# Performance work log

Measured on AMD Instinct MI355X. Metric: run time of the kernel, lower is better.

## Reference

```python
import math
import jax, jax.numpy as jnp
import numpy as np

D_MODEL = 1024
N_HEADS = 16
HEAD_DIM = D_MODEL // N_HEADS  # 64
QDIM = HEAD_DIM // 4           # 16
SPIKE_SLOPE = 5.0
B, S = 2, 2048


def _qweight(r, i, j, k):
    # Hamilton-product weight matrix, identical to QLinear.forward's torch.cat construction.
    return jnp.concatenate([
        jnp.concatenate([r, -i, -j, -k], 1),
        jnp.concatenate([i, r, -k, j], 1),
        jnp.concatenate([j, k, r, -i], 1),
        jnp.concatenate([k, -j, i, r], 1),
    ], 0)


def setup_inputs() -> dict:
    key = jax.random.key(0)
    ks = jax.random.split(key, 20)
    Qo = Qi = D_MODEL // 4  # 256
    p = lambda k, shape, s=0.02: (jax.random.normal(k, shape, dtype=jnp.float32) * s)
    inp = {
        'query': jax.random.normal(ks[0], (B, S, D_MODEL), dtype=jnp.float32),
        'key_in': jax.random.normal(ks[1], (B, S, D_MODEL), dtype=jnp.float32),
        'value': jax.random.normal(ks[2], (B, S, D_MODEL), dtype=jnp.float32),
        'mask': jnp.ones((B, S), dtype=jnp.int32),
        'density_feat': jax.random.normal(ks[3], (B, S, 3), dtype=jnp.float32),
        # q_proj QLinear params
        'wq_r': p(ks[4], (Qo, Qi)), 'wq_i': p(ks[5], (Qo, Qi)),
        'wq_j': p(ks[6], (Qo, Qi)), 'wq_k': p(ks[7], (Qo, Qi)),
        'bq': jnp.zeros((D_MODEL,), jnp.float32),
        # k_proj QLinear params
        'wk_r': p(ks[8], (Qo, Qi)), 'wk_i': p(ks[9], (Qo, Qi)),
        'wk_j': p(ks[10], (Qo, Qi)), 'wk_k': p(ks[11], (Qo, Qi)),
        'bk': jnp.zeros((D_MODEL,), jnp.float32),
        # v_proj / out_proj dense params
        'wv': p(ks[12], (D_MODEL, D_MODEL)), 'bv': jnp.zeros((D_MODEL,), jnp.float32),
        'wo': p(ks[13], (D_MODEL, D_MODEL)), 'bo': jnp.zeros((D_MODEL,), jnp.float32),
        # learned spike threshold (init -1.0 as in torch)
        'threshold': jnp.asarray(-1.0, dtype=jnp.float32),
        # density_mod MLP (use nonzero values so the gate shift is exercised)
        'dm1_w': p(ks[14], (16, 3), 0.5), 'dm1_b': p(ks[15], (16,), 0.1),
        'dm2_w': p(ks[16], (1, 16), 0.5), 'dm2_b': p(ks[17], (1,), 0.1),
    }
    return inp


def reference(query, key_in, value, mask, density_feat,
              wq_r, wq_i, wq_j, wq_k, bq,
              wk_r, wk_i, wk_j, wk_k, bk,
              wv, bv, wo, bo, threshold,
              dm1_w, dm1_b, dm2_w, dm2_b):
    H, hd, Qd = N_HEADS, HEAD_DIM, QDIM
    Bq, Sq, D = query.shape

    Wq = _qweight(wq_r, wq_i, wq_j, wq_k)
    Wk = _qweight(wk_r, wk_i, wk_j, wk_k)
    q = query @ Wq.T + bq
    k = key_in @ Wk.T + bk
    v = value @ wv.T + bv

    # head-major split, matching torch.cat(x.split(hd, -1), dim=0)
    qh = q.reshape(Bq, Sq, H, hd).transpose(2, 0, 1, 3)  # (H,B,S,hd)
    kh = k.reshape(Bq, Sq, H, hd).transpose(2, 0, 1, 3)
    vh = v.reshape(Bq, Sq, H, hd).transpose(2, 0, 1, 3)

    # sum of 4 quaternion-component dot products == full dot product over hd
    scores = jnp.einsum('hbmd,hbnd->hbmn', qh, kh) / math.sqrt(Qd)
    scores = jnp.clip(scores, -6.0, 6.0)

    base_threshold = jax.nn.softplus(threshold)
    h1 = jax.nn.gelu(density_feat @ dm1_w.T + dm1_b, approximate=False)
    d_shift = (h1 @ dm2_w.T + dm2_b)[..., 0]  # (B,N)
    thr = base_threshold + d_shift[None, :, None, :] * 0.1  # (1,B,1,N)

    spike_gate = jax.nn.sigmoid(SPIKE_SLOPE * (scores - thr))
    mod = scores * (1.0 + spike_gate * 2.0)

    m2 = (mask[:, :, None] * mask[:, None, :])[None]  # (1,B,N,N)
    mod = jnp.where(m2 == 0, -10000.0, mod)

    weights = jax.nn.softmax(jnp.clip(mod, -30.0, 30.0), axis=-1)
    # dropout: eval mode (identity)
    out_h = jnp.einsum('hbmn,hbnd->hbmd', weights, vh)
    out = out_h.transpose(1, 2, 0, 3).reshape(Bq, Sq, D)
    return out @ wo.T + bo
```

## Files before the change

kernel.cpp:

```cpp
#include <hip/hip_runtime.h>
#include <stdint.h>
#include <math.h>

#define BB 2
#define SS 2048
#define DM 1024
#define NH 16
#define HD 64
#define MTOT (BB*SS)

typedef __bf16 bf16x8 __attribute__((ext_vector_type(8)));
typedef float  f32x4  __attribute__((ext_vector_type(4)));
typedef uint32_t u32x4 __attribute__((ext_vector_type(4)));

__device__ __forceinline__ unsigned short f2bf(float f) {
  __bf16 h = (__bf16)f;
  return __builtin_bit_cast(unsigned short, h);
}

__device__ __forceinline__ bf16x8 ldsv8(const unsigned short* p) {
  return __builtin_bit_cast(bf16x8, *(const u32x4*)p);
}

__device__ __forceinline__ void gl16(const void* g, void* l) {
  __builtin_amdgcn_global_load_lds(
      (const __attribute__((address_space(1))) uint32_t*)g,
      (__attribute__((address_space(3))) uint32_t*)l, 16, 0, 0);
}

#define MFMA16(a,b,c) __builtin_amdgcn_mfma_f32_16x16x32_bf16((a),(b),(c),0,0,0)

#define C_NEG5L2E  (-7.213475204444817f)
#define C_L2E      (1.4426950408889634f)
#define C_18L2E    (25.968510736001341f)

__global__ __launch_bounds__(256) void prep_all(
    const float* __restrict__ wqr, const float* __restrict__ wqi,
    const float* __restrict__ wqj, const float* __restrict__ wqk,
    const float* __restrict__ wkr, const float* __restrict__ wki,
    const float* __restrict__ wkj, const float* __restrict__ wkk,
    const float* __restrict__ wv,  const float* __restrict__ wo,
    unsigned short* __restrict__ Wq, unsigned short* __restrict__ Wk,
    unsigned short* __restrict__ Wv, unsigned short* __restrict__ Wo,
    const float* __restrict__ query, const float* __restrict__ key_in,
    const float* __restrict__ value,
    unsigned short* __restrict__ qcv, unsigned short* __restrict__ kcv,
    unsigned short* __restrict__ vcv,
    const float* __restrict__ density, const float* __restrict__ dm1w,
    const float* __restrict__ dm1b, const float* __restrict__ dm2w,
    const float* __restrict__ dm2b, const float* __restrict__ thr_s,
    const int* __restrict__ mask, float2* __restrict__ klim)
{
  const int bid = blockIdx.x;
  if (bid < 512) {
    const int idx = (bid * 256 + threadIdx.x) * 8;
    const int o = idx >> 10, i = idx & 1023;
    const int br = o >> 8, bc = i >> 8;
    const int ro = o & 255, ci = i & 255;
    const int comp[4][4] = {{0,1,2,3},{1,0,3,2},{2,3,0,1},{3,2,1,0}};
    const float sgn[4][4] = {{1.f,-1.f,-1.f,-1.f},{1.f,1.f,-1.f,1.f},{1.f,1.f,1.f,-1.f},{1.f,-1.f,1.f,1.f}};
    const float* pq[4] = {wqr, wqi, wqj, wqk};
    const float* pk[4] = {wkr, wki, wkj, wkk};
    const int c_ = comp[br][bc];
    const float s_ = sgn[br][bc];
    const float* qsrc = pq[c_] + ro * 256 + ci;
    const float* ksrc = pk[c_] + ro * 256 + ci;
    {
      const float4 f0 = *(const float4*)qsrc;
      const float4 f1 = *(const float4*)(qsrc + 4);
      union { unsigned short us[8]; u32x4 v; } t;
      t.us[0]=f2bf(s_*f0.x); t.us[1]=f2bf(s_*f0.y); t.us[2]=f2bf(s_*f0.z); t.us[3]=f2bf(s_*f0.w);
      t.us[4]=f2bf(s_*f1.x); t.us[5]=f2bf(s_*f1.y); t.us[6]=f2bf(s_*f1.z); t.us[7]=f2bf(s_*f1.w);
      *(u32x4*)(Wq + idx) = t.v;
    }
    {
      const float4 f0 = *(const float4*)ksrc;
      const float4 f1 = *(const float4*)(ksrc + 4);
      union { unsigned short us[8]; u32x4 v; } t;
      t.us[0]=f2bf(s_*f0.x); t.us[1]=f2bf(s_*f0.y); t.us[2]=f2bf(s_*f0.z); t.us[3]=f2bf(s_*f0.w);
      t.us[4]=f2bf(s_*f1.x); t.us[5]=f2bf(s_*f1.y); t.us[6]=f2bf(s_*f1.z); t.us[7]=f2bf(s_*f1.w);
      *(u32x4*)(Wk + idx) = t.v;
    }
    {
      const float4 f0 = *(const float4*)(wv + idx);
      const float4 f1 = *(const float4*)(wv + idx + 4);
      union { unsigned short us[8]; u32x4 v; } t;
      t.us[0]=f2bf(f0.x); t.us[1]=f2bf(f0.y); t.us[2]=f2bf(f0.z); t.us[3]=f2bf(f0.w);
      t.us[4]=f2bf(f1.x); t.us[5]=f2bf(f1.y); t.us[6]=f2bf(f1.z); t.us[7]=f2bf(f1.w);
      *(u32x4*)(Wv + idx) = t.v;
    }
    {
      const float4 f0 = *(const float4*)(wo + idx);
      const float4 f1 = *(const float4*)(wo + idx + 4);
      union { unsigned short us[8]; u32x4 v; } t;
      t.us[0]=f2bf(f0.x); t.us[1]=f2bf(f0.y); t.us[2]=f2bf(f0.z); t.us[3]=f2bf(f0.w);
      t.us[4]=f2bf(f1.x); t.us[5]=f2bf(f1.y); t.us[6]=f2bf(f1.z); t.us[7]=f2bf(f1.w);
      *(u32x4*)(Wo + idx) = t.v;
    }
  } else if (bid < 2560) {
    const int i8 = ((bid - 512) * 256 + threadIdx.x) * 8;
    {
      const float4 f0 = *(const float4*)(query + i8);
      const float4 f1 = *(const float4*)(query + i8 + 4);
      union { unsigned short us[8]; u32x4 v; } t;
      t.us[0]=f2bf(f0.x); t.us[1]=f2bf(f0.y); t.us[2]=f2bf(f0.z); t.us[3]=f2bf(f0.w);
      t.us[4]=f2bf(f1.x); t.us[5]=f2bf(f1.y); t.us[6]=f2bf(f1.z); t.us[7]=f2bf(f1.w);
      *(u32x4*)(qcv + i8) = t.v;
    }
    {
      const float4 f0 = *(const float4*)(key_in + i8);
      const float4 f1 = *(const float4*)(key_in + i8 + 4);
      union { unsigned short us[8]; u32x4 v; } t;
      t.us[0]=f2bf(f0.x); t.us[1]=f2bf(f0.y); t.us[2]=f2bf(f0.z); t.us[3]=f2bf(f0.w);
      t.us[4]=f2bf(f1.x); t.us[5]=f2bf(f1.y); t.us[6]=f2bf(f1.z); t.us[7]=f2bf(f1.w);
      *(u32x4*)(kcv + i8) = t.v;
    }
    {
      const float4 f0 = *(const float4*)(value + i8);
      const float4 f1 = *(const float4*)(value + i8 + 4);
      union { unsigned short us[8]; u32x4 v; } t;
      t.us[0]=f2bf(f0.x); t.us[1]=f2bf(f0.y); t.us[2]=f2bf(f0.z); t.us[3]=f2bf(f0.w);
      t.us[4]=f2bf(f1.x); t.us[5]=f2bf(f1.y); t.us[6]=f2bf(f1.z); t.us[7]=f2bf(f1.w);
      *(u32x4*)(vcv + i8) = t.v;
    }
  } else {
    const int i = (bid - 2560) * 256 + threadIdx.x;
    if (i >= BB * SS) return;
    const float x0 = density[i*3+0], x1 = density[i*3+1], x2 = density[i*3+2];
    const float base = log1pf(expf(thr_s[0]));
    float acc = dm2b[0];
    #pragma unroll
    for (int j = 0; j < 16; ++j) {
      const float hj = dm1w[j*3+0]*x0 + dm1w[j*3+1]*x1 + dm1w[j*3+2]*x2 + dm1b[j];
      const float ge = 0.5f * hj * (1.0f + erff(hj * 0.70710678118654752f));
      acc += dm2w[j] * ge;
    }
    const float thr = base + 0.1f * acc;
    klim[i] = make_float2(thr * (-C_NEG5L2E),
                          mask[i] ? 1e30f : -30.0f);
  }
}

struct GemmArgs {
  const unsigned short* A[3];
  const unsigned short* W[3];
  const float* bias[3];
  void* out[3];
  float scale[3];
  int omode[3];
};

template<int DB>
__global__ __launch_bounds__(256) void gemm_bt(GemmArgs args)
{
  __shared__ __align__(16) unsigned short lA[DB + 1][128*64];
  __shared__ __align__(16) unsigned short lB[DB + 1][128*64];
  const int z = blockIdx.y;
  const int tid = threadIdx.x;
  const int wid = tid >> 6, lane = tid & 63;
  const int l15 = lane & 15, l4 = lane >> 4;
  const int bm = blockIdx.x & 31, bn = blockIdx.x >> 5;
  const int row0 = bm * 128, col0 = bn * 128;
  const int wm = (wid >> 1) * 64, wn = (wid & 1) * 64;

  const unsigned short* gA[4];
  const unsigned short* gB[4];
  #pragma unroll
  for (int i = 0; i < 4; ++i) {
    const int c = (wid * 4 + i) * 64 + lane;
    const int r = c >> 3, jx = c & 7, j = jx ^ (r & 7);
    gA[i] = args.A[z] + (row0 + r) * 1024 + j * 8;
    gB[i] = args.W[z] + (col0 + r) * 1024 + j * 8;
  }

  f32x4 acc[4][4];
  #pragma unroll
  for (int i = 0; i < 4; ++i)
    #pragma unroll
    for (int j = 0; j < 4; ++j) acc[i][j] = (f32x4){0.f,0.f,0.f,0.f};

  #pragma unroll
  for (int i = 0; i < 4; ++i) {
    gl16(gA[i], &lA[0][(wid * 4 + i) * 512]);
    gl16(gB[i], &lB[0][(wid * 4 + i) * 512]);
  }
  if (DB) __syncthreads();

  for (int kt = 0; kt < 16; ++kt) {
    const int cb = DB ? (kt & 1) : 0;
    if (DB) {
      if (kt < 15) {
        const int nb = cb ^ 1, k0 = (kt + 1) * 64;
        #pragma unroll
        for (int i = 0; i < 4; ++i) {
          gl16(gA[i] + k0, &lA[nb][(wid * 4 + i) * 512]);
          gl16(gB[i] + k0, &lB[nb][(wid * 4 + i) * 512]);
        }
      }
    } else {
      if (kt > 0) {
        const int k0 = kt * 64;
        #pragma unroll
        for (int i = 0; i < 4; ++i) {
          gl16(gA[i] + k0, &lA[0][(wid * 4 + i) * 512]);
          gl16(gB[i] + k0, &lB[0][(wid * 4 + i) * 512]);
        }
      }
      __syncthreads();
    }
    #pragma unroll
    for (int kk = 0; kk < 2; ++kk) {
      const int kl = kk * 32 + l4 * 8;
      bf16x8 af[4], bfb[4];
      #pragma unroll
      for (int mi = 0; mi < 4; ++mi) {
        const int r = wm + mi * 16 + l15;
        af[mi] = ldsv8(&lA[cb][r * 64 + (kl ^ ((r & 7) << 3))]);
      }
      #pragma unroll
      for (int nj = 0; nj < 4; ++nj) {
        const int r = wn + nj * 16 + l15;
        bfb[nj] = ldsv8(&lB[cb][r * 64 + (kl ^ ((r & 7) << 3))]);
      }
      #pragma unroll
      for (int mi = 0; mi < 4; ++mi)
        #pragma unroll
        for (int nj = 0; nj < 4; ++nj)
          acc[mi][nj] = MFMA16(af[mi], bfb[nj], acc[mi][nj]);
    }
    __syncthreads();
  }

  const int om = args.omode[z];
  const float sc = args.scale[z];
  void* Cptr = args.out[z];
  #pragma unroll
  for (int nj = 0; nj < 4; ++nj) {
    const int c = col0 + wn + nj * 16 + l15;
    const float bv_ = args.bias[z][c];
    #pragma unroll
    for (int mi = 0; mi < 4; ++mi) {
      const int rb = row0 + wm + mi * 16 + l4 * 4;
      #pragma unroll
      for (int e = 0; e < 4; ++e) {
        const float val = (acc[mi][nj][e] + bv_) * sc;
        const int r = rb + e;
        if (om == 0) {
          ((unsigned short*)Cptr)[r * 1024 + c] = f2bf(val);
        } else if (om == 2) {
          ((float*)Cptr)[r * 1024 + c] = val;
        } else {
          const int h = c >> 6, d = c & 63, b = r >> 11, s = r & 2047;
          ((unsigned short*)Cptr)[((h * BB + b) * HD + d) * SS + s] = f2bf(val);
        }
      }
    }
  }
}

__global__ __launch_bounds__(512) void attn_kernel(
    const unsigned short* __restrict__ qg, const unsigned short* __restrict__ kg,
    const unsigned short* __restrict__ vT, const float2* __restrict__ klim,
    const int* __restrict__ mask, unsigned short* __restrict__ outg)
{
  __shared__ __align__(16) unsigned short smem[20480];
  unsigned short* lK = smem;
  unsigned short* lV = smem + 8192;
  unsigned short* lP = smem + 16384;

  const int tid = threadIdx.x;
  const int wid = tid >> 6, lane = tid & 63;
  const int l15 = lane & 15, l4 = lane >> 4;
  const int rg = wid >> 1, par = wid & 1;
  const int hb = blockIdx.x & 31, qb = blockIdx.x >> 5;
  const int h = hb >> 1, b = hb & 1;
  const int qr0 = qb * 64 + rg * 16;

  const int kcr = tid >> 3, kcj = (tid & 7) * 8;
  const int vcd = tid >> 3, vck = (tid & 7) * 8;
  const int kdst = (kcr >> 5) * 2048 + (kcr & 31) * 64 + (kcj ^ ((((kcr & 31) >> 1) & 7) << 3));
  const int vdst = (vck >> 5) * 2048 + vcd * 32 + ((vck & 31) ^ ((vcd & 3) << 3));

  const unsigned short* kbase = kg + (b * SS) * DM + h * HD;
  const unsigned short* vbase = vT + ((h * BB + b) * HD) * SS;
  const float2* klimb = klim + b * SS;

  bf16x8 aq[2];
  {
    const unsigned short* qs = qg + (b * SS + qr0 + l15) * DM + h * HD + l4 * 8;
    aq[0] = __builtin_bit_cast(bf16x8, *(const u32x4*)qs);
    aq[1] = __builtin_bit_cast(bf16x8, *(const u32x4*)(qs + 32));
  }
  float limq[4];
  #pragma unroll
  for (int e = 0; e < 4; ++e)
    limq[e] = mask[b * SS + qr0 + l4 * 4 + e] ? 1e30f : -30.0f;

  float lrun[4] = {0.f, 0.f, 0.f, 0.f};
  f32x4 o[4];
  #pragma unroll
  for (int d = 0; d < 4; ++d) o[d] = (f32x4){0.f,0.f,0.f,0.f};

  unsigned short* lPw = lP + wid * 512;

  u32x4 kr = *(const u32x4*)(kbase + kcr * DM + kcj);
  u32x4 vr = *(const u32x4*)(vbase + vcd * SS + vck);
  *(u32x4*)&lK[kdst] = kr;
  *(u32x4*)&lV[vdst] = vr;
  __syncthreads();

  for (int pr = 0; pr < 32; ++pr) {
    const int cur = pr & 1;
    const unsigned short* lKt = lK + cur * 4096 + par * 2048;
    const unsigned short* lVt = lV + cur * 4096 + par * 2048;
    const int n0 = pr * 64 + par * 32;

    if (pr < 31) {
      const int nn = (pr + 1) * 64;
      kr = *(const u32x4*)(kbase + (nn + kcr) * DM + kcj);
      vr = *(const u32x4*)(vbase + vcd * SS + nn + vck);
    }

    const float4 klA = *(const float4*)(klimb + n0 + 2 * l15);

    f32x4 sv[2];
    __builtin_amdgcn_s_setprio(1);
    #pragma unroll
    for (int cf = 0; cf < 2; ++cf) {
      f32x4 a = (f32x4){0.f,0.f,0.f,0.f};
      const int r = 2 * l15 + cf;
      #pragma unroll
      for (int kk = 0; kk < 2; ++kk)
        a = MFMA16(aq[kk], ldsv8(&lKt[r * 64 + ((kk * 32 + l4 * 8) ^ ((l15 & 7) << 3))]), a);
      sv[cf] = a;
    }
    __builtin_amdgcn_s_setprio(0);

    float pvv[2][4];
    #pragma unroll
    for (int cf = 0; cf < 2; ++cf) {
      const float kth = cf ? klA.z : klA.x;
      const float klm = cf ? klA.w : klA.y;
      #pragma unroll
      for (int e = 0; e < 4; ++e) {
        float s = fminf(fmaxf(sv[cf][e], -6.f), 6.f);
        const float t = __builtin_amdgcn_exp2f(fmaf(s, C_NEG5L2E, kth));
        const float g = __builtin_amdgcn_rcpf(1.f + t);
        float md = fmaf(s + s, g, s);
        md = fminf(md, fminf(klm, limq[e]));
        const float p = __builtin_amdgcn_exp2f(fmaf(md, C_L2E, -C_18L2E));
        pvv[cf][e] = p;
        lrun[e] += p;
      }
    }

    #pragma unroll
    for (int e = 0; e < 4; ++e) {
      const int rr = l4 * 4 + e;
      union { unsigned short us[2]; unsigned int u; } pk2;
      pk2.us[0] = f2bf(pvv[0][e]);
      pk2.us[1] = f2bf(pvv[1][e]);
      *(unsigned int*)&lPw[rr * 32 + ((2 * l15) ^ ((rr & 3) << 3))] = pk2.u;
    }
    asm volatile("s_waitcnt lgkmcnt(0)" ::: "memory");
    __builtin_amdgcn_sched_barrier(0);

    const bf16x8 pa = ldsv8(&lPw[l15 * 32 + ((l4 * 8) ^ ((l15 & 3) << 3))]);

    __builtin_amdgcn_s_setprio(1);
    #pragma unroll
    for (int df = 0; df < 4; ++df) {
      const int d = df * 16 + l15;
      o[df] = MFMA16(pa, ldsv8(&lVt[d * 32 + ((l4 * 8) ^ ((d & 3) << 3))]), o[df]);
    }
    __builtin_amdgcn_s_setprio(0);

    if (pr < 31) {
      const int nxt = cur ^ 1;
      *(u32x4*)&lK[nxt * 4096 + kdst] = kr;
      *(u32x4*)&lV[nxt * 4096 + vdst] = vr;
    }
    __syncthreads();
  }

  __syncthreads();
  float* xch = (float*)smem;
  float* slot = xch + rg * 1280;
  if (par) {
    #pragma unroll
    for (int df = 0; df < 4; ++df)
      *(f32x4*)&slot[(df * 64 + lane) * 4] = o[df];
    f32x4 lr;
    lr[0] = lrun[0]; lr[1] = lrun[1]; lr[2] = lrun[2]; lr[3] = lrun[3];
    *(f32x4*)&slot[1024 + lane * 4] = lr;
  }
  __syncthreads();
  if (!par) {
    #pragma unroll
    for (int df = 0; df < 4; ++df) {
      const f32x4 t = *(const f32x4*)&slot[(df * 64 + lane) * 4];
      o[df][0] += t[0]; o[df][1] += t[1]; o[df][2] += t[2]; o[df][3] += t[3];
    }
    const f32x4 lr = *(const f32x4*)&slot[1024 + lane * 4];
    #pragma unroll
    for (int e = 0; e < 4; ++e) {
      float ls = lrun[e] + lr[e];
      ls += __shfl_xor(ls, 1);
      ls += __shfl_xor(ls, 2);
      ls += __shfl_xor(ls, 4);
      ls += __shfl_xor(ls, 8);
      const float rl = __builtin_amdgcn_rcpf(ls);
      const int r = qr0 + l4 * 4 + e;
      #pragma unroll
      for (int df = 0; df < 4; ++df) {
        outg[(b * SS + r) * DM + h * HD + df * 16 + l15] = f2bf(o[df][e] * rl);
      }
    }
  }
}

extern "C" void kernel_launch(void* const* d_in, const int* in_sizes, int n_in,
                              void* d_out, int out_size, void* d_ws, size_t ws_size,
                              hipStream_t stream)
{
  const float* query   = (const float*)d_in[0];
  const float* key_in  = (const float*)d_in[1];
  const float* value   = (const float*)d_in[2];
  const int*   mask    = (const int*)d_in[3];
  const float* density = (const float*)d_in[4];
  const float* wq_r = (const float*)d_in[5];
  const float* wq_i = (const float*)d_in[6];
  const float* wq_j = (const float*)d_in[7];
  const float* wq_k = (const float*)d_in[8];
  const float* bq   = (const float*)d_in[9];
  const float* wk_r = (const float*)d_in[10];
  const float* wk_i = (const float*)d_in[11];
  const float* wk_j = (const float*)d_in[12];
  const float* wk_k = (const float*)d_in[13];
  const float* bk   = (const float*)d_in[14];
  const float* wv   = (const float*)d_in[15];
  const float* bv   = (const float*)d_in[16];
  const float* wo   = (const float*)d_in[17];
  const float* bo   = (const float*)d_in[18];
  const float* thrs = (const float*)d_in[19];
  const float* dm1w = (const float*)d_in[20];
  const float* dm1b = (const float*)d_in[21];
  const float* dm2w = (const float*)d_in[22];
  const float* dm2b = (const float*)d_in[23];

  char* ws = (char*)d_ws;
  unsigned short* Wq  = (unsigned short*)(ws + ((size_t)0 << 20));
  unsigned short* Wk  = (unsigned short*)(ws + ((size_t)2 << 20));
  unsigned short* Wv  = (unsigned short*)(ws + ((size_t)4 << 20));
  unsigned short* Wo  = (unsigned short*)(ws + ((size_t)6 << 20));
  unsigned short* qbf = (unsigned short*)(ws + ((size_t)8 << 20));
  unsigned short* kbf = (unsigned short*)(ws + ((size_t)16 << 20));
  unsigned short* vT  = (unsigned short*)(ws + ((size_t)24 << 20));
  unsigned short* att = (unsigned short*)(ws + ((size_t)32 << 20));
  float2* klim        = (float2*)(ws + ((size_t)40 << 20));

  unsigned short* qcv = (unsigned short*)d_out;
  unsigned short* kcv = (unsigned short*)d_out + (size_t)MTOT * DM;
  unsigned short* vcv = att;

  prep_all<<<2576, 256, 0, stream>>>(
      wq_r, wq_i, wq_j, wq_k, wk_r, wk_i, wk_j, wk_k, wv, wo,
      Wq, Wk, Wv, Wo,
      query, key_in, value, qcv, kcv, vcv,
      density, dm1w, dm1b, dm2w, dm2b, thrs, mask, klim);

  GemmArgs qkv;
  qkv.A[0] = qcv; qkv.W[0] = Wq; qkv.bias[0] = bq; qkv.out[0] = qbf; qkv.scale[0] = 0.25f; qkv.omode[0] = 0;
  qkv.A[1] = kcv; qkv.W[1] = Wk; qkv.bias[1] = bk; qkv.out[1] = kbf; qkv.scale[1] = 1.0f;  qkv.omode[1] = 0;
  qkv.A[2] = vcv; qkv.W[2] = Wv; qkv.bias[2] = bv; qkv.out[2] = vT;  qkv.scale[2] = 1.0f;  qkv.omode[2] = 1;
  gemm_bt<0><<<dim3(256, 3), 256, 0, stream>>>(qkv);

  attn_kernel<<<1024, 512, 0, stream>>>(qbf, kbf, vT, klim, mask, att);

  GemmArgs og;
  og.A[0] = att; og.W[0] = Wo; og.bias[0] = bo; og.out[0] = d_out; og.scale[0] = 1.0f; og.omode[0] = 2;
  og.A[1] = att; og.W[1] = Wo; og.bias[1] = bo; og.out[1] = d_out; og.scale[1] = 1.0f; og.omode[1] = 2;
  og.A[2] = att; og.W[2] = Wo; og.bias[2] = bo; og.out[2] = d_out; og.scale[2] = 1.0f; og.omode[2] = 2;
  gemm_bt<1><<<dim3(256, 1), 256, 0, stream>>>(og);
}
```

Before: 182.1 us.

## Use direct global-to-LDS K/V loads and skip masking when batch mask is all ones

The attention kernel now streams K and V tiles straight into LDS with async global-to-LDS loads (gl16), using a per-wave pre-swizzled source address. This replaces the register-staged load-then-store double buffering and frees registers. The prep kernel also records, per batch, whether any mask entry is zero, and the attention kernel takes a cheaper softmax path without mask clamps when the batch is clean. The mask check is a runtime test rather than an assumption, but it adds a memset and atomics, and the loop is now unrolled by two.

```diff
diff --git a/kernel.cpp b/kernel.cpp
--- a/kernel.cpp
+++ b/kernel.cpp
@@ -49,7 +49,8 @@
     const float* __restrict__ density, const float* __restrict__ dm1w,
     const float* __restrict__ dm1b, const float* __restrict__ dm2w,
     const float* __restrict__ dm2b, const float* __restrict__ thr_s,
-    const int* __restrict__ mask, float2* __restrict__ klim)
+    const int* __restrict__ mask, float2* __restrict__ klim,
+    int* __restrict__ amask)
 {
   const int bid = blockIdx.x;
   if (bid < 512) {
@@ -136,8 +137,12 @@
       acc += dm2w[j] * ge;
     }
     const float thr = base + 0.1f * acc;
+    const int mk = mask[i];
     klim[i] = make_float2(thr * (-C_NEG5L2E),
-                          mask[i] ? 1e30f : -30.0f);
+                          mk ? 1e30f : -30.0f);
+    const unsigned long long any = __ballot(mk == 0);
+    if ((threadIdx.x & 63) == 0 && any)
+      atomicOr(&amask[i >> 11], 1);
   }
 }
 
@@ -261,9 +266,11 @@
 __global__ __launch_bounds__(512) void attn_kernel(
     const unsigned short* __restrict__ qg, const unsigned short* __restrict__ kg,
     const unsigned short* __restrict__ vT, const float2* __restrict__ klim,
-    const int* __restrict__ mask, unsigned short* __restrict__ outg)
+    const int* __restrict__ mask, const int* __restrict__ amask,
+    unsigned short* __restrict__ outg)
 {
   __shared__ __align__(16) unsigned short smem[20480];
+  unsigned char* sb = (unsigned char*)smem;
   unsigned short* lK = smem;
   unsigned short* lV = smem + 8192;
   unsigned short* lP = smem + 16384;
@@ -276,14 +283,21 @@
   const int h = hb >> 1, b = hb & 1;
   const int qr0 = qb * 64 + rg * 16;
 
-  const int kcr = tid >> 3, kcj = (tid & 7) * 8;
-  const int vcd = tid >> 3, vck = (tid & 7) * 8;
-  const int kdst = (kcr >> 5) * 2048 + (kcr & 31) * 64 + (kcj ^ ((((kcr & 31) >> 1) & 7) << 3));
-  const int vdst = (vck >> 5) * 2048 + vcd * 32 + ((vck & 31) ^ ((vcd & 3) << 3));
-
   const unsigned short* kbase = kg + (b * SS) * DM + h * HD;
   const unsigned short* vbase = vT + ((h * BB + b) * HD) * SS;
   const float2* klimb = klim + b * SS;
+  const int clean = (amask[b] == 0);
+
+  const int kp   = wid >> 2;
+  const int krho = ((wid & 3) << 3) | (lane >> 3);
+  const int kj   = (lane & 7) ^ ((krho >> 1) & 7);
+  const unsigned short* ksrc = kbase + (kp * 32 + krho) * DM + kj * 8;
+  const int vq   = wid >> 2;
+  const int vd   = ((wid & 3) << 4) | (lane >> 2);
+  const int vc   = (lane & 3) ^ (vd & 3);
+  const unsigned short* vsrc = vbase + (size_t)vd * SS + vq * 32 + vc * 8;
+  unsigned char* kdw = sb + wid * 1024;
+  unsigned char* vdw = sb + 16384 + wid * 1024;
 
   bf16x8 aq[2];
   {
@@ -292,9 +306,11 @@
     aq[1] = __builtin_bit_cast(bf16x8, *(const u32x4*)(qs + 32));
   }
   float limq[4];
-  #pragma unroll
-  for (int e = 0; e < 4; ++e)
-    limq[e] = mask[b * SS + qr0 + l4 * 4 + e] ? 1e30f : -30.0f;
+  if (!clean) {
+    #pragma unroll
+    for (int e = 0; e < 4; ++e)
+      limq[e] = mask[b * SS + qr0 + l4 * 4 + e] ? 1e30f : -30.0f;
+  }
 
   float lrun[4] = {0.f, 0.f, 0.f, 0.f};
   f32x4 o[4];
@@ -303,12 +319,11 @@
 
   unsigned short* lPw = lP + wid * 512;
 
-  u32x4 kr = *(const u32x4*)(kbase + kcr * DM + kcj);
-  u32x4 vr = *(const u32x4*)(vbase + vcd * SS + vck);
-  *(u32x4*)&lK[kdst] = kr;
-  *(u32x4*)&lV[vdst] = vr;
+  gl16(ksrc, kdw);
+  gl16(vsrc, vdw);
   __syncthreads();
 
+  #pragma unroll 2
   for (int pr = 0; pr < 32; ++pr) {
     const int cur = pr & 1;
     const unsigned short* lKt = lK + cur * 4096 + par * 2048;
@@ -316,9 +331,9 @@
     const int n0 = pr * 64 + par * 32;
 
     if (pr < 31) {
-      const int nn = (pr + 1) * 64;
-      kr = *(const u32x4*)(kbase + (nn + kcr) * DM + kcj);
-      vr = *(const u32x4*)(vbase + vcd * SS + nn + vck);
+      const int nxt = cur ^ 1;
+      gl16(ksrc + (size_t)(pr + 1) * 64 * DM, kdw + nxt * 8192);
+      gl16(vsrc + (pr + 1) * 64,              vdw + nxt * 8192);
     }
 
     const float4 klA = *(const float4*)(klimb + n0 + 2 * l15);
@@ -337,20 +352,37 @@
     __builtin_amdgcn_s_setprio(0);
 
     float pvv[2][4];
-    #pragma unroll
-    for (int cf = 0; cf < 2; ++cf) {
-      const float kth = cf ? klA.z : klA.x;
-      const float klm = cf ? klA.w : klA.y;
-      #pragma unroll
-      for (int e = 0; e < 4; ++e) {
-        float s = fminf(fmaxf(sv[cf][e], -6.f), 6.f);
-        const float t = __builtin_amdgcn_exp2f(fmaf(s, C_NEG5L2E, kth));
-        const float g = __builtin_amdgcn_rcpf(1.f + t);
-        float md = fmaf(s + s, g, s);
-        md = fminf(md, fminf(klm, limq[e]));
-        const float p = __builtin_amdgcn_exp2f(fmaf(md, C_L2E, -C_18L2E));
-        pvv[cf][e] = p;
-        lrun[e] += p;
+    if (clean) {
+      #pragma unroll
+      for (int cf = 0; cf < 2; ++cf) {
+        const float kth = cf ? klA.z : klA.x;
+        #pragma unroll
+        for (int e = 0; e < 4; ++e) {
+          float s = fminf(fmaxf(sv[cf][e], -6.f), 6.f);
+          const float t = __builtin_amdgcn_exp2f(fmaf(s, C_NEG5L2E, kth));
+          const float g = __builtin_amdgcn_rcpf(1.f + t);
+          const float md = fmaf(s + s, g, s);
+          const float p = __builtin_amdgcn_exp2f(fmaf(md, C_L2E, -C_18L2E));
+          pvv[cf][e] = p;
+          lrun[e] += p;
+        }
+      }
+    } else {
+      #pragma unroll
+      for (int cf = 0; cf < 2; ++cf) {
+        const float kth = cf ? klA.z : klA.x;
+        const float klm = cf ? klA.w : klA.y;
+        #pragma unroll
+        for (int e = 0; e < 4; ++e) {
+          float s = fminf(fmaxf(sv[cf][e], -6.f), 6.f);
+          const float t = __builtin_amdgcn_exp2f(fmaf(s, C_NEG5L2E, kth));
+          const float g = __builtin_amdgcn_rcpf(1.f + t);
+          float md = fmaf(s + s, g, s);
+          md = fminf(md, fminf(klm, limq[e]));
+          const float p = __builtin_amdgcn_exp2f(fmaf(md, C_L2E, -C_18L2E));
+          pvv[cf][e] = p;
+          lrun[e] += p;
+        }
       }
     }
 
@@ -375,11 +407,6 @@
     }
     __builtin_amdgcn_s_setprio(0);
 
-    if (pr < 31) {
-      const int nxt = cur ^ 1;
-      *(u32x4*)&lK[nxt * 4096 + kdst] = kr;
-      *(u32x4*)&lV[nxt * 4096 + vdst] = vr;
-    }
     __syncthreads();
   }
 
@@ -458,16 +485,18 @@
   unsigned short* vT  = (unsigned short*)(ws + ((size_t)24 << 20));
   unsigned short* att = (unsigned short*)(ws + ((size_t)32 << 20));
   float2* klim        = (float2*)(ws + ((size_t)40 << 20));
+  int* amask          = (int*)(ws + ((size_t)40 << 20) + 65536);
 
   unsigned short* qcv = (unsigned short*)d_out;
   unsigned short* kcv = (unsigned short*)d_out + (size_t)MTOT * DM;
   unsigned short* vcv = att;
 
+  hipMemsetAsync(amask, 0, 2 * sizeof(int), stream);
   prep_all<<<2576, 256, 0, stream>>>(
       wq_r, wq_i, wq_j, wq_k, wk_r, wk_i, wk_j, wk_k, wv, wo,
       Wq, Wk, Wv, Wo,
       query, key_in, value, qcv, kcv, vcv,
-      density, dm1w, dm1b, dm2w, dm2b, thrs, mask, klim);
+      density, dm1w, dm1b, dm2w, dm2b, thrs, mask, klim, amask);
 
   GemmArgs qkv;
   qkv.A[0] = qcv; qkv.W[0] = Wq; qkv.bias[0] = bq; qkv.out[0] = qbf; qkv.scale[0] = 0.25f; qkv.omode[0] = 0;
@@ -475,7 +504,7 @@
   qkv.A[2] = vcv; qkv.W[2] = Wv; qkv.bias[2] = bv; qkv.out[2] = vT;  qkv.scale[2] = 1.0f;  qkv.omode[2] = 1;
   gemm_bt<0><<<dim3(256, 3), 256, 0, stream>>>(qkv);
 
-  attn_kernel<<<1024, 512, 0, stream>>>(qbf, kbf, vT, klim, mask, att);
+  attn_kernel<<<1024, 512, 0, stream>>>(qbf, kbf, vT, klim, mask, amask, att);
 
   GemmArgs og;
   og.A[0] = att; og.W[0] = Wo; og.bias[0] = bo; og.out[0] = d_out; og.scale[0] = 1.0f; og.omode[0] = 2;
```

After: 185.1 us. Within noise of the previous version (+1.6%).
